# Performance work log

Measured on AMD Instinct MI355X. Metric: run time of the kernel, lower is better.

## Reference

```python
import jax, jax.numpy as jnp
import numpy as np

N_LAYERS = 8
WIDTH = 1024
N = N_LAYERS * WIDTH


def setup_inputs() -> dict:
    key = jax.random.key(0)
    k1, k2 = jax.random.split(key)
    x = jax.random.normal(k1, (WIDTH,), dtype=jnp.float32)
    # parameter_matrix: row i = weights over all N neurons + bias in column N
    params = jax.random.normal(k2, (N, N + 1), dtype=jnp.float32) * 0.1
    # Layered DAG adjacency: layer l -> layer l+1 fully connected.
    adj_np = np.zeros((N, N), dtype=bool)
    for l in range(N_LAYERS - 1):
        adj_np[l * WIDTH:(l + 1) * WIDTH, (l + 1) * WIDTH:(l + 2) * WIDTH] = True
    return {"x": x, "params": params, "adj": jnp.asarray(adj_np)}


def reference(x, params, adj):
    """Faithful forward of connex NeuralNetwork with dropout_p=0.

    values starts at zero; input neurons (ids 0..W-1) are set to x.
    Each topological batch (= layer here) fires via the dense masked
    dot-product the original uses: dot(params[i,:N], values*adj[:,i]) + bias.
    Hidden neurons use silu, output neurons use identity.
    """
    n = params.shape[0]
    w = x.shape[0]
    n_layers = n // w
    values = jnp.zeros((n,), dtype=x.dtype).at[:w].set(x)
    for l in range(1, n_layers):  # static loop over topo batches
        lo, hi = l * w, (l + 1) * w
        mask = adj[:, lo:hi].T                      # (w, n) incoming-edge mask
        masked = jnp.where(mask, values[None, :], 0.0)
        pre = jnp.einsum('wn,wn->w', params[lo:hi, :n], masked) + params[lo:hi, n]
        out = pre if l == n_layers - 1 else jax.nn.silu(pre)  # output_activation = identity
        values = values.at[lo:hi].set(out)
    return values[-w:]
```

## Files before the change

### kernel.cpp

```cpp
#include <hip/hip_runtime.h>
#include <math.h>

#define W_    1024
#define NL_   8
#define NTOT_ (W_ * NL_)
#define RS_   (NTOT_ + 1)
#define NBLK  256

typedef unsigned long long u64;

__device__ __forceinline__ u64 ld64(const u64* p) {
    return __hip_atomic_load(p, __ATOMIC_RELAXED, __HIP_MEMORY_SCOPE_AGENT);
}
__device__ __forceinline__ void st64(u64* p, u64 v) {
    __hip_atomic_store(p, v, __ATOMIC_RELAXED, __HIP_MEMORY_SCOPE_AGENT);
}
__device__ __forceinline__ u64 pack(int tag, float v) {
    return ((u64)(unsigned)tag << 32) | (u64)__float_as_uint(v);
}

__global__ __launch_bounds__(256, 1)
void mlp_fused(const float* __restrict__ x, const float* __restrict__ params,
               float* __restrict__ out, float* __restrict__ ws) {
    __shared__ float h[W_];
    const int tid  = threadIdx.x;
    const int lane = tid & 63;
    const int wave = tid >> 6;
    const int row  = blockIdx.x * 4 + wave;

    u64* bufs[2] = { (u64*)ws, (u64*)ws + W_ };

    float bias[NL_ - 1];
#pragma unroll
    for (int l = 1; l < NL_; ++l)
        bias[l - 1] = params[(size_t)(l * W_ + row) * RS_ + NTOT_];

    float wreg[2][16];
    {
        const float* wrow = params + (size_t)(1 * W_ + row) * RS_ + lane;
#pragma unroll
        for (int i = 0; i < 16; ++i) wreg[0][i] = wrow[64 * i];
    }

#pragma unroll
    for (int i = 0; i < 4; ++i) h[tid + 256 * i] = x[tid + 256 * i];
    __syncthreads();

#pragma unroll
    for (int l = 1; l < NL_; ++l) {
        if (l < NL_ - 1) {
            const float* wrow = params + (size_t)((l + 1) * W_ + row) * RS_
                                       + (size_t)l * W_ + lane;
#pragma unroll
            for (int i = 0; i < 16; ++i) wreg[l & 1][i] = wrow[64 * i];
        }

        if (l > 1) {
            const u64* cur = bufs[l & 1];
            const u64 want = (u64)(unsigned)(l - 1);
            u64 u0, u1, u2, u3;
            do {
                u0 = ld64(cur + tid);
                u1 = ld64(cur + tid + 256);
                u2 = ld64(cur + tid + 512);
                u3 = ld64(cur + tid + 768);
            } while (((u0 >> 32) != want) | ((u1 >> 32) != want) |
                     ((u2 >> 32) != want) | ((u3 >> 32) != want));
            h[tid]       = __uint_as_float((unsigned)u0);
            h[tid + 256] = __uint_as_float((unsigned)u1);
            h[tid + 512] = __uint_as_float((unsigned)u2);
            h[tid + 768] = __uint_as_float((unsigned)u3);
            __syncthreads();
        }

        float acc = 0.f;
#pragma unroll
        for (int i = 0; i < 16; ++i)
            acc += wreg[(l - 1) & 1][i] * h[lane + 64 * i];
#pragma unroll
        for (int off = 32; off; off >>= 1)
            acc += __shfl_down(acc, off);

        if (lane == 0) {
            float pre = acc + bias[l - 1];
            if (l == NL_ - 1) out[row] = pre;
            else {
                float v = pre / (1.f + __expf(-pre));
                st64(bufs[(l - 1) & 1] + row, pack(l, v));
            }
        }
    }
}

extern "C" void kernel_launch(void* const* d_in, const int* in_sizes, int n_in,
                              void* d_out, int out_size, void* d_ws, size_t ws_size,
                              hipStream_t stream) {
    const float* x      = (const float*)d_in[0];
    const float* params = (const float*)d_in[1];
    float* out = (float*)d_out;
    float* ws  = (float*)d_ws;

    hipLaunchKernelGGL(mlp_fused, dim3(NBLK), dim3(256), 0, stream,
                       x, params, out, ws);
}
```

Measured before the change: 410.7 us.

## Replace block barrier with per-wave polling and prefetch all layer weights

After: 421.4 us. +2.6%, slower.

```diff
diff --git a/kernel.cpp b/kernel.cpp
--- a/kernel.cpp
+++ b/kernel.cpp
@@ -22,7 +22,6 @@
 __global__ __launch_bounds__(256, 1)
 void mlp_fused(const float* __restrict__ x, const float* __restrict__ params,
                float* __restrict__ out, float* __restrict__ ws) {
-    __shared__ float h[W_];
     const int tid  = threadIdx.x;
     const int lane = tid & 63;
     const int wave = tid >> 6;
@@ -30,64 +29,57 @@
 
     u64* bufs[2] = { (u64*)ws, (u64*)ws + W_ };
 
+    float vreg[16];
+#pragma unroll
+    for (int i = 0; i < 16; ++i) vreg[i] = x[lane + 64 * i];
+
     float bias[NL_ - 1];
 #pragma unroll
     for (int l = 1; l < NL_; ++l)
         bias[l - 1] = params[(size_t)(l * W_ + row) * RS_ + NTOT_];
 
-    float wreg[2][16];
-    {
-        const float* wrow = params + (size_t)(1 * W_ + row) * RS_ + lane;
+    float wreg[NL_ - 1][16];
 #pragma unroll
-        for (int i = 0; i < 16; ++i) wreg[0][i] = wrow[64 * i];
+    for (int l = 1; l < NL_; ++l) {
+        const float* wrow = params + (size_t)(l * W_ + row) * RS_
+                                   + (size_t)(l - 1) * W_ + lane;
+#pragma unroll
+        for (int i = 0; i < 16; ++i) wreg[l - 1][i] = wrow[64 * i];
     }
 
 #pragma unroll
-    for (int i = 0; i < 4; ++i) h[tid + 256 * i] = x[tid + 256 * i];
-    __syncthreads();
-
-#pragma unroll
     for (int l = 1; l < NL_; ++l) {
-        if (l < NL_ - 1) {
-            const float* wrow = params + (size_t)((l + 1) * W_ + row) * RS_
-                                       + (size_t)l * W_ + lane;
-#pragma unroll
-            for (int i = 0; i < 16; ++i) wreg[l & 1][i] = wrow[64 * i];
-        }
-
-        if (l > 1) {
-            const u64* cur = bufs[l & 1];
-            const u64 want = (u64)(unsigned)(l - 1);
-            u64 u0, u1, u2, u3;
-            do {
-                u0 = ld64(cur + tid);
-                u1 = ld64(cur + tid + 256);
-                u2 = ld64(cur + tid + 512);
-                u3 = ld64(cur + tid + 768);
-            } while (((u0 >> 32) != want) | ((u1 >> 32) != want) |
-                     ((u2 >> 32) != want) | ((u3 >> 32) != want));
-            h[tid]       = __uint_as_float((unsigned)u0);
-            h[tid + 256] = __uint_as_float((unsigned)u1);
-            h[tid + 512] = __uint_as_float((unsigned)u2);
-            h[tid + 768] = __uint_as_float((unsigned)u3);
-            __syncthreads();
-        }
-
         float acc = 0.f;
 #pragma unroll
         for (int i = 0; i < 16; ++i)
-            acc += wreg[(l - 1) & 1][i] * h[lane + 64 * i];
+            acc += wreg[l - 1][i] * vreg[i];
 #pragma unroll
         for (int off = 32; off; off >>= 1)
             acc += __shfl_down(acc, off);
 
-        if (lane == 0) {
-            float pre = acc + bias[l - 1];
-            if (l == NL_ - 1) out[row] = pre;
-            else {
+        if (l == NL_ - 1) {
+            if (lane == 0) out[row] = acc + bias[l - 1];
+        } else {
+            if (lane == 0) {
+                float pre = acc + bias[l - 1];
                 float v = pre / (1.f + __expf(-pre));
                 st64(bufs[(l - 1) & 1] + row, pack(l, v));
             }
+            const u64* cur = bufs[(l - 1) & 1];
+            const unsigned want = (unsigned)l;
+            u64 u[16];
+            for (;;) {
+#pragma unroll
+                for (int i = 0; i < 16; ++i) u[i] = ld64(cur + lane + 64 * i);
+                bool ok = true;
+#pragma unroll
+                for (int i = 0; i < 16; ++i)
+                    ok &= ((unsigned)(u[i] >> 32) == want);
+                if (ok) break;
+            }
+#pragma unroll
+            for (int i = 0; i < 16; ++i)
+                vreg[i] = __uint_as_float((unsigned)u[i]);
         }
     }
 }
```
